# Optimization experiments

Hardware: AMD Instinct MI355X
Metric: run time of the kernel (lower is better)

## Reference

```python
import jax, jax.numpy as jnp
import numpy as np

HIDDEN = 4096
FFN = 11008
N_HEADS = 32
HEAD_DIM = HIDDEN // N_HEADS
BATCH = 1
SEQLEN = 1024
PAST = 1024
ROPE_BASE = 10000.0
EPS = 1e-6


def rms_norm(x, w, eps=EPS):
    var = jnp.mean(x * x, axis=-1, keepdims=True)
    return x * jax.lax.rsqrt(var + eps) * w


def rope(x):
    # x: (b, h, s, d); concatenated-halves variant: [e*cos - o*sin, e*sin + o*cos]
    s, d = x.shape[-2], x.shape[-1]
    pos = jnp.arange(s, dtype=x.dtype)[:, None]                      # (s, 1)
    freqs = ROPE_BASE ** (-jnp.arange(0, d, 2, dtype=x.dtype) / d)   # (d/2,)
    ang = pos * freqs                                                # (s, d/2)
    cos, sin = jnp.cos(ang), jnp.sin(ang)
    xe, xo = x[..., ::2], x[..., 1::2]
    return jnp.concatenate([xe * cos - xo * sin, xe * sin + xo * cos], axis=-1)


def setup_inputs() -> dict:
    key = jax.random.key(0)
    ks = jax.random.split(key, 9)
    sc = 0.02
    return {
        "x": jax.random.normal(ks[0], (BATCH, SEQLEN, HIDDEN), jnp.float32),
        "wq": jax.random.normal(ks[1], (HIDDEN, HIDDEN), jnp.float32) * sc,
        "wk": jax.random.normal(ks[2], (HIDDEN, HIDDEN), jnp.float32) * sc,
        "wv": jax.random.normal(ks[3], (HIDDEN, HIDDEN), jnp.float32) * sc,
        "wo": jax.random.normal(ks[4], (HIDDEN, HIDDEN), jnp.float32) * sc,
        "w1": jax.random.normal(ks[5], (FFN, HIDDEN), jnp.float32) * sc,
        "w2": jax.random.normal(ks[6], (HIDDEN, FFN), jnp.float32) * sc,
        "w3": jax.random.normal(ks[7], (FFN, HIDDEN), jnp.float32) * sc,
        "attn_norm_w": jnp.ones((HIDDEN,), jnp.float32),
        "ffn_norm_w": jnp.ones((HIDDEN,), jnp.float32),
        "past_k": jnp.zeros((BATCH, N_HEADS, PAST, HEAD_DIM), jnp.float32),
        "past_v": jnp.zeros((BATCH, N_HEADS, PAST, HEAD_DIM), jnp.float32),
    }


def reference(x, wq, wk, wv, wo, w1, w2, w3, attn_norm_w, ffn_norm_w, past_k, past_v):
    bsz, seqlen, _ = x.shape
    h = rms_norm(x, attn_norm_w)
    # projections: nn.Linear -> h @ W^T, reshape to (b, n_heads, s, d)
    def split_heads(y):
        return y.reshape(bsz, seqlen, N_HEADS, HEAD_DIM).transpose(0, 2, 1, 3)
    xq = split_heads(h @ wq.T)
    xk = split_heads(h @ wk.T)
    xv = split_heads(h @ wv.T)
    xq = rope(xq)
    xk = rope(xk)  # computed but unused downstream (faithful to source)
    # attention against the KV-cache buffers (zeros); no scaling, no mask
    scores_raw = jnp.einsum('bhsd,bhpd->bhsp', xq, past_k)
    scores = jax.nn.softmax(scores_raw, axis=-1)
    out = jnp.einsum('bhsp,bhpd->bhsd', scores, past_v)
    out = out.transpose(0, 2, 1, 3).reshape(bsz, seqlen, -1)
    xo = out @ wo.T
    # SwiGLU FFN (no residuals in source)
    hf = rms_norm(xo, ffn_norm_w)
    x1 = hf @ w1.T
    x3 = jax.nn.silu(hf @ w3.T)
    return (x1 * x3) @ w2.T
```

## Files before the change

kernel.cpp:

```cpp
#include <hip/hip_runtime.h>
#include <hip/hip_bf16.h>


typedef __attribute__((ext_vector_type(4))) float  floatx4;
typedef __attribute__((ext_vector_type(8))) __bf16 bf16x8;
typedef __attribute__((ext_vector_type(4))) __bf16 bf16x4;

#define HIDDEN 4096
#define FFN    11008
#define SEQLEN 1024
#define NHEADS 32
#define HDIM   128
#define PAST   1024

__global__ __launch_bounds__(256) void rmsnorm_bf16(
    const float* __restrict__ x, const float* __restrict__ w,
    __bf16* __restrict__ out)
{
    const int row = blockIdx.x;
    const float* xr = x + (size_t)row * HIDDEN;
    float4 v[4];
    float ss = 0.f;
#pragma unroll
    for (int i = 0; i < 4; ++i) {
        v[i] = *(const float4*)(xr + threadIdx.x * 4 + i * 1024);
        ss += v[i].x * v[i].x + v[i].y * v[i].y + v[i].z * v[i].z + v[i].w * v[i].w;
    }
#pragma unroll
    for (int off = 32; off > 0; off >>= 1) ss += __shfl_down(ss, off);
    __shared__ float red[4];
    if ((threadIdx.x & 63) == 0) red[threadIdx.x >> 6] = ss;
    __syncthreads();
    float total = red[0] + red[1] + red[2] + red[3];
    float scale = rsqrtf(total * (1.f / HIDDEN) + 1e-6f);
#pragma unroll
    for (int i = 0; i < 4; ++i) {
        int idx = threadIdx.x * 4 + i * 1024;
        float4 wv = *(const float4*)(w + idx);
        bf16x4 o;
        o[0] = (__bf16)(v[i].x * scale * wv.x);
        o[1] = (__bf16)(v[i].y * scale * wv.y);
        o[2] = (__bf16)(v[i].z * scale * wv.z);
        o[3] = (__bf16)(v[i].w * scale * wv.w);
        *(bf16x4*)(out + (size_t)row * HIDDEN + idx) = o;
    }
}

__global__ __launch_bounds__(256) void gemm_bt(
    const __bf16* __restrict__ A, const float* __restrict__ W,
    float* __restrict__ C, int M, int N, int K)
{
    __shared__ __bf16 As[128][40];
    __shared__ __bf16 Bs[128][40];

    const int tid  = threadIdx.x;
    const int bn   = blockIdx.x;
    const int bm   = blockIdx.y;
    const int wave = tid >> 6;
    const int lane = tid & 63;
    const int wr   = wave >> 1;
    const int wc   = wave & 1;
    const int lrow = lane & 15;
    const int quad = lane >> 4;

    floatx4 acc[4][4] = {};

    for (int k0 = 0; k0 < K; k0 += 32) {
#pragma unroll
        for (int i = 0; i < 2; ++i) {
            int id = tid + i * 256;
            int r = id >> 2, cc = id & 3;
            bf16x8 av = *(const bf16x8*)(A + (size_t)(bm * 128 + r) * K + k0 + cc * 8);
            *(bf16x8*)(&As[r][cc * 8]) = av;
        }
#pragma unroll
        for (int i = 0; i < 4; ++i) {
            int id = tid + i * 256;
            int r = id >> 3, cc = id & 7;
            float4 wv = *(const float4*)(W + (size_t)(bn * 128 + r) * K + k0 + cc * 4);
            bf16x4 bv;
            bv[0] = (__bf16)wv.x; bv[1] = (__bf16)wv.y;
            bv[2] = (__bf16)wv.z; bv[3] = (__bf16)wv.w;
            *(bf16x4*)(&Bs[r][cc * 4]) = bv;
        }
        __syncthreads();

        bf16x8 af[4], bfr[4];
#pragma unroll
        for (int i = 0; i < 4; ++i)
            af[i] = *(const bf16x8*)(&As[wr * 64 + i * 16 + lrow][quad * 8]);
#pragma unroll
        for (int j = 0; j < 4; ++j)
            bfr[j] = *(const bf16x8*)(&Bs[wc * 64 + j * 16 + lrow][quad * 8]);
#pragma unroll
        for (int i = 0; i < 4; ++i)
#pragma unroll
            for (int j = 0; j < 4; ++j)
                acc[i][j] = __builtin_amdgcn_mfma_f32_16x16x32_bf16(af[i], bfr[j], acc[i][j], 0, 0, 0);
        __syncthreads();
    }

#pragma unroll
    for (int i = 0; i < 4; ++i) {
        int mrow = bm * 128 + wr * 64 + i * 16 + quad * 4;
#pragma unroll
        for (int j = 0; j < 4; ++j) {
            int ncol = bn * 128 + wc * 64 + j * 16 + lrow;
            float* cp = C + (size_t)mrow * N + ncol;
#pragma unroll
            for (int r = 0; r < 4; ++r)
                cp[(size_t)r * N] = acc[i][j][r];
        }
    }
}

__global__ __launch_bounds__(256) void rope_cast(
    const float* __restrict__ xq, __bf16* __restrict__ outq)
{
    const int s = blockIdx.x;
    const float* row = xq + (size_t)s * HIDDEN;
    __bf16* orow = outq + (size_t)s * HIDDEN;
    for (int idx = threadIdx.x; idx < HIDDEN; idx += 256) {
        int d = idx & 127;
        int j = d & 63;
        int base = idx - d;
        float xe = row[base + 2 * j];
        float xo = row[base + 2 * j + 1];
        float freq = __powf(10000.f, -(float)(2 * j) * (1.f / 128.f));
        float sn, cs;
        __sincosf((float)s * freq, &sn, &cs);
        float v = (d < 64) ? (xe * cs - xo * sn) : (xe * sn + xo * cs);
        orow[idx] = (__bf16)v;
    }
}

__global__ __launch_bounds__(256) void attn_flash(
    const __bf16* __restrict__ q, const float* __restrict__ pk,
    const float* __restrict__ pv, __bf16* __restrict__ out)
{
    const int qt = blockIdx.x;
    const int h  = blockIdx.y;
    const int s0 = qt * 64;
    const int tid  = threadIdx.x;
    const int wave = tid >> 6;
    const int lane = tid & 63;
    const int l15  = lane & 15;
    const int quad = lane >> 4;

    __shared__ __bf16 Ks[64 * 136];
    __shared__ __bf16 Vt[128 * 72];
    __shared__ __bf16 Ps[64 * 72];

    bf16x8 qf[4];
    {
        const __bf16* qrow = q + (size_t)(s0 + wave * 16 + l15) * HIDDEN + h * HDIM;
#pragma unroll
        for (int ks = 0; ks < 4; ++ks)
            qf[ks] = *(const bf16x8*)(qrow + ks * 32 + quad * 8);
    }

    floatx4 Oa[8] = {};
    float m_r[4], l_r[4];
#pragma unroll
    for (int r = 0; r < 4; ++r) { m_r[r] = -1e30f; l_r[r] = 0.f; }

    for (int p0 = 0; p0 < PAST; p0 += 64) {
        const float* kbase = pk + ((size_t)h * PAST + p0) * HDIM;
        const float* vbase = pv + ((size_t)h * PAST + p0) * HDIM;
#pragma unroll
        for (int i = 0; i < 8; ++i) {
            int f = i * 256 + tid;
            int p = f >> 5, dq = (f & 31) * 4;
            float4 k4 = *(const float4*)(kbase + p * HDIM + dq);
            bf16x4 kb;
            kb[0] = (__bf16)k4.x; kb[1] = (__bf16)k4.y;
            kb[2] = (__bf16)k4.z; kb[3] = (__bf16)k4.w;
            *(bf16x4*)(&Ks[p * 136 + dq]) = kb;
            float4 v4 = *(const float4*)(vbase + p * HDIM + dq);
            Vt[(dq + 0) * 72 + p] = (__bf16)v4.x;
            Vt[(dq + 1) * 72 + p] = (__bf16)v4.y;
            Vt[(dq + 2) * 72 + p] = (__bf16)v4.z;
            Vt[(dq + 3) * 72 + p] = (__bf16)v4.w;
        }
        __syncthreads();

        floatx4 Sa[4] = {};
#pragma unroll
        for (int nb = 0; nb < 4; ++nb)
#pragma unroll
            for (int ks = 0; ks < 4; ++ks) {
                bf16x8 kf = *(const bf16x8*)(&Ks[(nb * 16 + l15) * 136 + ks * 32 + quad * 8]);
                Sa[nb] = __builtin_amdgcn_mfma_f32_16x16x32_bf16(qf[ks], kf, Sa[nb], 0, 0, 0);
            }

        float mnew[4];
#pragma unroll
        for (int r = 0; r < 4; ++r) {
            float t = fmaxf(fmaxf(Sa[0][r], Sa[1][r]), fmaxf(Sa[2][r], Sa[3][r]));
#pragma unroll
            for (int off = 1; off < 16; off <<= 1) t = fmaxf(t, __shfl_xor(t, off));
            mnew[r] = fmaxf(m_r[r], t);
        }
#pragma unroll
        for (int r = 0; r < 4; ++r) {
            float alpha = __expf(m_r[r] - mnew[r]);
            m_r[r] = mnew[r];
            float s = 0.f;
#pragma unroll
            for (int nb = 0; nb < 4; ++nb) {
                float e = __expf(Sa[nb][r] - mnew[r]);
                Sa[nb][r] = e;
                s += e;
            }
#pragma unroll
            for (int off = 1; off < 16; off <<= 1) s += __shfl_xor(s, off);
            l_r[r] = l_r[r] * alpha + s;
#pragma unroll
            for (int nb = 0; nb < 8; ++nb) Oa[nb][r] *= alpha;
        }

#pragma unroll
        for (int nb = 0; nb < 4; ++nb)
#pragma unroll
            for (int r = 0; r < 4; ++r)
                Ps[(wave * 16 + quad * 4 + r) * 72 + nb * 16 + l15] = (__bf16)Sa[nb][r];

#pragma unroll
        for (int ks2 = 0; ks2 < 2; ++ks2) {
            bf16x8 pf = *(const bf16x8*)(&Ps[(wave * 16 + l15) * 72 + ks2 * 32 + quad * 8]);
#pragma unroll
            for (int nb = 0; nb < 8; ++nb) {
                bf16x8 vf = *(const bf16x8*)(&Vt[(nb * 16 + l15) * 72 + ks2 * 32 + quad * 8]);
                Oa[nb] = __builtin_amdgcn_mfma_f32_16x16x32_bf16(pf, vf, Oa[nb], 0, 0, 0);
            }
        }
        __syncthreads();
    }

    float inv[4];
#pragma unroll
    for (int r = 0; r < 4; ++r) inv[r] = 1.f / l_r[r];
#pragma unroll
    for (int nb = 0; nb < 8; ++nb)
#pragma unroll
        for (int r = 0; r < 4; ++r)
            out[(size_t)(s0 + wave * 16 + quad * 4 + r) * HIDDEN + h * HDIM + nb * 16 + l15] =
                (__bf16)(Oa[nb][r] * inv[r]);
}

__global__ __launch_bounds__(256) void silu_mul_bf16(
    const float* __restrict__ x1, const float* __restrict__ x3,
    __bf16* __restrict__ out)
{
    int i = (blockIdx.x * 256 + threadIdx.x) * 4;
    float4 a = *(const float4*)(x1 + i);
    float4 b = *(const float4*)(x3 + i);
    bf16x4 o;
    o[0] = (__bf16)(a.x * (b.x / (1.f + __expf(-b.x))));
    o[1] = (__bf16)(a.y * (b.y / (1.f + __expf(-b.y))));
    o[2] = (__bf16)(a.z * (b.z / (1.f + __expf(-b.z))));
    o[3] = (__bf16)(a.w * (b.w / (1.f + __expf(-b.w))));
    *(bf16x4*)(out + i) = o;
}

extern "C" void kernel_launch(void* const* d_in, const int* in_sizes, int n_in,
                              void* d_out, int out_size, void* d_ws, size_t ws_size,
                              hipStream_t stream)
{
    const float* x   = (const float*)d_in[0];
    const float* wq  = (const float*)d_in[1];
    const float* wo  = (const float*)d_in[4];
    const float* w1  = (const float*)d_in[5];
    const float* w2  = (const float*)d_in[6];
    const float* w3  = (const float*)d_in[7];
    const float* anw = (const float*)d_in[8];
    const float* fnw = (const float*)d_in[9];
    const float* pk  = (const float*)d_in[10];
    const float* pv  = (const float*)d_in[11];
    float* out = (float*)d_out;

    char* ws = (char*)d_ws;
    constexpr size_t MB = 1ull << 20;
    __bf16* h_bf  = (__bf16*)(ws);
    float*  xq    = (float*)(ws + 8 * MB);
    __bf16* xq_bf = (__bf16*)(ws + 24 * MB);
    __bf16* ao_bf = (__bf16*)(ws + 32 * MB);
    float*  xo    = (float*)(ws + 40 * MB);
    __bf16* hf_bf = (__bf16*)(ws + 56 * MB);
    float*  x1    = (float*)(ws + 64 * MB);
    float*  x3    = (float*)(ws + 108 * MB);
    __bf16* g_bf  = (__bf16*)(ws + 152 * MB);

    rmsnorm_bf16<<<SEQLEN, 256, 0, stream>>>(x, anw, h_bf);
    gemm_bt<<<dim3(HIDDEN / 128, SEQLEN / 128), 256, 0, stream>>>(h_bf, wq, xq, SEQLEN, HIDDEN, HIDDEN);
    rope_cast<<<SEQLEN, 256, 0, stream>>>(xq, xq_bf);
    attn_flash<<<dim3(SEQLEN / 64, NHEADS), 256, 0, stream>>>(xq_bf, pk, pv, ao_bf);
    gemm_bt<<<dim3(HIDDEN / 128, SEQLEN / 128), 256, 0, stream>>>(ao_bf, wo, xo, SEQLEN, HIDDEN, HIDDEN);
    rmsnorm_bf16<<<SEQLEN, 256, 0, stream>>>(xo, fnw, hf_bf);
    gemm_bt<<<dim3(FFN / 128, SEQLEN / 128), 256, 0, stream>>>(hf_bf, w1, x1, SEQLEN, FFN, HIDDEN);
    gemm_bt<<<dim3(FFN / 128, SEQLEN / 128), 256, 0, stream>>>(hf_bf, w3, x3, SEQLEN, FFN, HIDDEN);
    silu_mul_bf16<<<(SEQLEN * FFN) / 1024, 256, 0, stream>>>(x1, x3, g_bf);
    gemm_bt<<<dim3(HIDDEN / 128, SEQLEN / 128), 256, 0, stream>>>(g_bf, w2, out, SEQLEN, HIDDEN, FFN);
}
```

Baseline: 1.682 ms.

## Double-buffer GEMM with direct-to-LDS loads, split-K, XCD remap, and RoPE table

Replaces the GEMM kernel with a K=64, double-buffered version. The A tile streams straight into LDS through global_load_lds with an XOR swizzle, while the next W tile is prefetched into registers during the MFMA work. Workgroups are remapped across XCDs. The 4096-wide GEMMs use a two-way split-K, and new combine kernels sum the partials (fused with RoPE for Q). RoPE sin/cos is precomputed into a table. The split-K path adds extra fp32 partial writes and reads in exchange for more parallelism and better latency hiding.

```diff
diff --git a/kernel.cpp b/kernel.cpp
--- a/kernel.cpp
+++ b/kernel.cpp
@@ -12,6 +12,12 @@
 #define NHEADS 32
 #define HDIM   128
 #define PAST   1024
+
+__device__ __forceinline__ void gload_lds16(const void* g, void* l) {
+    __builtin_amdgcn_global_load_lds(
+        (const __attribute__((address_space(1))) void*)g,
+        (__attribute__((address_space(3))) void*)l, 16, 0, 0);
+}
 
 __global__ __launch_bounds__(256) void rmsnorm_bf16(
     const float* __restrict__ x, const float* __restrict__ w,
@@ -46,92 +52,171 @@
     }
 }
 
-__global__ __launch_bounds__(256) void gemm_bt(
+template<int SPLIT>
+__global__ __launch_bounds__(256, 2) void gemm2(
     const __bf16* __restrict__ A, const float* __restrict__ W,
     float* __restrict__ C, int M, int N, int K)
 {
-    __shared__ __bf16 As[128][40];
-    __shared__ __bf16 Bs[128][40];
+    __shared__ __bf16 Asb[2][128 * 64];
+    __shared__ __bf16 Bsb[2][128 * 72];
 
     const int tid  = threadIdx.x;
-    const int bn   = blockIdx.x;
-    const int bm   = blockIdx.y;
     const int wave = tid >> 6;
     const int lane = tid & 63;
+    const int l15  = lane & 15;
+    const int quad = lane >> 4;
     const int wr   = wave >> 1;
     const int wc   = wave & 1;
-    const int lrow = lane & 15;
-    const int quad = lane >> 4;
+
+    const int nwg = gridDim.x;
+    int flat = blockIdx.x;
+    int q = nwg >> 3, r = nwg & 7;
+    int xcd = flat & 7, ii = flat >> 3;
+    int nf = (xcd < r) ? (xcd * (q + 1) + ii) : (r * (q + 1) + (xcd - r) * q + ii);
+    const int gm = M >> 7;
+    const int bn = nf / gm, bm = nf - bn * gm;
+
+    const int Kper  = K / SPLIT;
+    const int kbase = blockIdx.y * Kper;
+    const int nt    = Kper >> 6;
+
+    const int arow = (lane >> 3);
+    const int akb  = ((lane & 7) * 16) ^ ((lane >> 3) << 4);
+    const __bf16* Abase = A + (size_t)(bm * 128) * K + kbase + (akb >> 1);
+
+    const int wrow = tid >> 1, wh = tid & 1;
+    const float* Wbase = W + (size_t)(bn * 128 + wrow) * K + kbase + wh * 32;
 
     floatx4 acc[4][4] = {};
-
-    for (int k0 = 0; k0 < K; k0 += 32) {
-#pragma unroll
-        for (int i = 0; i < 2; ++i) {
-            int id = tid + i * 256;
-            int r = id >> 2, cc = id & 3;
-            bf16x8 av = *(const bf16x8*)(A + (size_t)(bm * 128 + r) * K + k0 + cc * 8);
-            *(bf16x8*)(&As[r][cc * 8]) = av;
-        }
+    float4 wreg[8];
+
+    {
+#pragma unroll
+        for (int j = 0; j < 8; ++j)
+            wreg[j] = *(const float4*)(Wbase + j * 4);
 #pragma unroll
         for (int i = 0; i < 4; ++i) {
-            int id = tid + i * 256;
-            int r = id >> 3, cc = id & 7;
-            float4 wv = *(const float4*)(W + (size_t)(bn * 128 + r) * K + k0 + cc * 4);
-            bf16x4 bv;
-            bv[0] = (__bf16)wv.x; bv[1] = (__bf16)wv.y;
-            bv[2] = (__bf16)wv.z; bv[3] = (__bf16)wv.w;
-            *(bf16x4*)(&Bs[r][cc * 4]) = bv;
+            int c = wave * 4 + i;
+            gload_lds16(Abase + (size_t)(c * 8 + arow) * K, &Asb[0][c * 512]);
+        }
+#pragma unroll
+        for (int j = 0; j < 4; ++j) {
+            bf16x8 b;
+            b[0] = (__bf16)wreg[2*j].x;   b[1] = (__bf16)wreg[2*j].y;
+            b[2] = (__bf16)wreg[2*j].z;   b[3] = (__bf16)wreg[2*j].w;
+            b[4] = (__bf16)wreg[2*j+1].x; b[5] = (__bf16)wreg[2*j+1].y;
+            b[6] = (__bf16)wreg[2*j+1].z; b[7] = (__bf16)wreg[2*j+1].w;
+            *(bf16x8*)(&Bsb[0][wrow * 72 + wh * 32 + j * 8]) = b;
         }
         __syncthreads();
-
-        bf16x8 af[4], bfr[4];
-#pragma unroll
-        for (int i = 0; i < 4; ++i)
-            af[i] = *(const bf16x8*)(&As[wr * 64 + i * 16 + lrow][quad * 8]);
-#pragma unroll
-        for (int j = 0; j < 4; ++j)
-            bfr[j] = *(const bf16x8*)(&Bs[wc * 64 + j * 16 + lrow][quad * 8]);
-#pragma unroll
-        for (int i = 0; i < 4; ++i)
-#pragma unroll
-            for (int j = 0; j < 4; ++j)
-                acc[i][j] = __builtin_amdgcn_mfma_f32_16x16x32_bf16(af[i], bfr[j], acc[i][j], 0, 0, 0);
-        __syncthreads();
-    }
-
+    }
+
+    for (int t = 0; t < nt; ++t) {
+        const int cur = t & 1, nxt = cur ^ 1;
+        const bool more = (t + 1 < nt);
+
+        if (more) {
+            const float* wb = Wbase + (t + 1) * 64;
+#pragma unroll
+            for (int j = 0; j < 8; ++j)
+                wreg[j] = *(const float4*)(wb + j * 4);
+            const __bf16* ab = Abase + (t + 1) * 64;
+#pragma unroll
+            for (int i = 0; i < 4; ++i) {
+                int c = wave * 4 + i;
+                gload_lds16(ab + (size_t)(c * 8 + arow) * K, &Asb[nxt][c * 512]);
+            }
+        }
+
+#pragma unroll
+        for (int kk = 0; kk < 2; ++kk) {
+            bf16x8 af[4], bfr[4];
+#pragma unroll
+            for (int i = 0; i < 4; ++i) {
+                int R  = wr * 64 + i * 16 + l15;
+                int kb = (kk * 64 + quad * 16) ^ ((l15 & 7) << 4);
+                af[i] = *(const bf16x8*)((const char*)&Asb[cur][R * 64] + kb);
+            }
+#pragma unroll
+            for (int j = 0; j < 4; ++j) {
+                int R2 = wc * 64 + j * 16 + l15;
+                bfr[j] = *(const bf16x8*)(&Bsb[cur][R2 * 72 + kk * 32 + quad * 8]);
+            }
+#pragma unroll
+            for (int i = 0; i < 4; ++i)
+#pragma unroll
+                for (int j = 0; j < 4; ++j)
+                    acc[i][j] = __builtin_amdgcn_mfma_f32_16x16x32_bf16(af[i], bfr[j], acc[i][j], 0, 0, 0);
+        }
+
+        if (more) {
+#pragma unroll
+            for (int j = 0; j < 4; ++j) {
+                bf16x8 b;
+                b[0] = (__bf16)wreg[2*j].x;   b[1] = (__bf16)wreg[2*j].y;
+                b[2] = (__bf16)wreg[2*j].z;   b[3] = (__bf16)wreg[2*j].w;
+                b[4] = (__bf16)wreg[2*j+1].x; b[5] = (__bf16)wreg[2*j+1].y;
+                b[6] = (__bf16)wreg[2*j+1].z; b[7] = (__bf16)wreg[2*j+1].w;
+                *(bf16x8*)(&Bsb[nxt][wrow * 72 + wh * 32 + j * 8]) = b;
+            }
+            __syncthreads();
+        }
+    }
+
+    float* Co = (SPLIT > 1) ? (C + (size_t)blockIdx.y * M * N) : C;
 #pragma unroll
     for (int i = 0; i < 4; ++i) {
         int mrow = bm * 128 + wr * 64 + i * 16 + quad * 4;
 #pragma unroll
         for (int j = 0; j < 4; ++j) {
-            int ncol = bn * 128 + wc * 64 + j * 16 + lrow;
-            float* cp = C + (size_t)mrow * N + ncol;
-#pragma unroll
-            for (int r = 0; r < 4; ++r)
-                cp[(size_t)r * N] = acc[i][j][r];
-        }
-    }
-}
-
-__global__ __launch_bounds__(256) void rope_cast(
-    const float* __restrict__ xq, __bf16* __restrict__ outq)
+            int ncol = bn * 128 + wc * 64 + j * 16 + l15;
+            float* cp = Co + (size_t)mrow * N + ncol;
+#pragma unroll
+            for (int rr = 0; rr < 4; ++rr)
+                cp[(size_t)rr * N] = acc[i][j][rr];
+        }
+    }
+}
+
+__global__ __launch_bounds__(256) void rope_table(float* __restrict__ tab)
+{
+    int idx = blockIdx.x * 256 + threadIdx.x;
+    int s = idx >> 6, j = idx & 63;
+    float freq = __powf(10000.f, -(float)(2 * j) * (1.f / 128.f));
+    float sn, cs;
+    __sincosf((float)s * freq, &sn, &cs);
+    tab[2 * idx]     = cs;
+    tab[2 * idx + 1] = sn;
+}
+
+__global__ __launch_bounds__(256) void combine_rope(
+    const float* __restrict__ p, const float* __restrict__ tab,
+    __bf16* __restrict__ out)
 {
     const int s = blockIdx.x;
-    const float* row = xq + (size_t)s * HIDDEN;
-    __bf16* orow = outq + (size_t)s * HIDDEN;
-    for (int idx = threadIdx.x; idx < HIDDEN; idx += 256) {
-        int d = idx & 127;
-        int j = d & 63;
-        int base = idx - d;
-        float xe = row[base + 2 * j];
-        float xo = row[base + 2 * j + 1];
-        float freq = __powf(10000.f, -(float)(2 * j) * (1.f / 128.f));
-        float sn, cs;
-        __sincosf((float)s * freq, &sn, &cs);
-        float v = (d < 64) ? (xe * cs - xo * sn) : (xe * sn + xo * cs);
-        orow[idx] = (__bf16)v;
-    }
+    const float* r0 = p + (size_t)s * HIDDEN;
+    const float* r1 = r0 + (size_t)SEQLEN * HIDDEN;
+    __bf16* orow = out + (size_t)s * HIDDEN;
+    for (int pi = threadIdx.x; pi < 2048; pi += 256) {
+        int h = pi >> 6, j = pi & 63;
+        int base = h * 128;
+        float2 e0 = *(const float2*)(r0 + base + 2 * j);
+        float2 e1 = *(const float2*)(r1 + base + 2 * j);
+        float xe = e0.x + e1.x, xo = e0.y + e1.y;
+        float2 cs = *(const float2*)(tab + (size_t)s * 128 + 2 * j);
+        orow[base + j]      = (__bf16)(xe * cs.x - xo * cs.y);
+        orow[base + 64 + j] = (__bf16)(xe * cs.y + xo * cs.x);
+    }
+}
+
+__global__ __launch_bounds__(256) void combine_add(
+    const float* __restrict__ p, float* __restrict__ out, int n)
+{
+    int i = (blockIdx.x * 256 + threadIdx.x) * 4;
+    float4 a = *(const float4*)(p + i);
+    float4 b = *(const float4*)(p + n + i);
+    float4 o; o.x = a.x + b.x; o.y = a.y + b.y; o.z = a.z + b.z; o.w = a.w + b.w;
+    *(float4*)(out + i) = o;
 }
 
 __global__ __launch_bounds__(256) void attn_flash(
@@ -280,25 +365,37 @@
     float* out = (float*)d_out;
 
     char* ws = (char*)d_ws;
-    constexpr size_t MB = 1ull << 20;
-    __bf16* h_bf  = (__bf16*)(ws);
-    float*  xq    = (float*)(ws + 8 * MB);
-    __bf16* xq_bf = (__bf16*)(ws + 24 * MB);
-    __bf16* ao_bf = (__bf16*)(ws + 32 * MB);
-    float*  xo    = (float*)(ws + 40 * MB);
-    __bf16* hf_bf = (__bf16*)(ws + 56 * MB);
-    float*  x1    = (float*)(ws + 64 * MB);
-    float*  x3    = (float*)(ws + 108 * MB);
-    __bf16* g_bf  = (__bf16*)(ws + 152 * MB);
-
+    constexpr size_t MB  = 1ull << 20;
+    constexpr size_t HMB = 512ull << 10;
+    float*  tab   = (float*)(ws);
+    __bf16* h_bf  = (__bf16*)(ws + HMB);
+    float*  qp    = (float*)(ws + HMB + 8  * MB);
+    __bf16* xq_bf = (__bf16*)(ws + HMB);
+    __bf16* ao_bf = (__bf16*)(ws + HMB + 8  * MB);
+    float*  op    = (float*)(ws + HMB + 16 * MB);
+    float*  xo    = (float*)(ws + HMB);
+    __bf16* hf_bf = (__bf16*)(ws + HMB + 48 * MB);
+    float*  x1    = (float*)(ws + HMB);
+    float*  x3    = (float*)(ws + HMB + 56 * MB);
+    __bf16* g_bf  = (__bf16*)(ws + HMB + 102 * MB);
+    float*  w2p   = (float*)(ws + HMB);
+
+    rope_table<<<256, 256, 0, stream>>>(tab);
     rmsnorm_bf16<<<SEQLEN, 256, 0, stream>>>(x, anw, h_bf);
-    gemm_bt<<<dim3(HIDDEN / 128, SEQLEN / 128), 256, 0, stream>>>(h_bf, wq, xq, SEQLEN, HIDDEN, HIDDEN);
-    rope_cast<<<SEQLEN, 256, 0, stream>>>(xq, xq_bf);
+    gemm2<2><<<dim3((HIDDEN / 128) * (SEQLEN / 128), 2), 256, 0, stream>>>(
+        h_bf, wq, qp, SEQLEN, HIDDEN, HIDDEN);
+    combine_rope<<<SEQLEN, 256, 0, stream>>>(qp, tab, xq_bf);
     attn_flash<<<dim3(SEQLEN / 64, NHEADS), 256, 0, stream>>>(xq_bf, pk, pv, ao_bf);
-    gemm_bt<<<dim3(HIDDEN / 128, SEQLEN / 128), 256, 0, stream>>>(ao_bf, wo, xo, SEQLEN, HIDDEN, HIDDEN);
+    gemm2<2><<<dim3((HIDDEN / 128) * (SEQLEN / 128), 2), 256, 0, stream>>>(
+        ao_bf, wo, op, SEQLEN, HIDDEN, HIDDEN);
+    combine_add<<<(SEQLEN * HIDDEN) / 1024, 256, 0, stream>>>(op, xo, SEQLEN * HIDDEN);
     rmsnorm_bf16<<<SEQLEN, 256, 0, stream>>>(xo, fnw, hf_bf);
-    gemm_bt<<<dim3(FFN / 128, SEQLEN / 128), 256, 0, stream>>>(hf_bf, w1, x1, SEQLEN, FFN, HIDDEN);
-    gemm_bt<<<dim3(FFN / 128, SEQLEN / 128), 256, 0, stream>>>(hf_bf, w3, x3, SEQLEN, FFN, HIDDEN);
+    gemm2<1><<<dim3((FFN / 128) * (SEQLEN / 128), 1), 256, 0, stream>>>(
+        hf_bf, w1, x1, SEQLEN, FFN, HIDDEN);
+    gemm2<1><<<dim3((FFN / 128) * (SEQLEN / 128), 1), 256, 0, stream>>>(
+        hf_bf, w3, x3, SEQLEN, FFN, HIDDEN);
     silu_mul_bf16<<<(SEQLEN * FFN) / 1024, 256, 0, stream>>>(x1, x3, g_bf);
-    gemm_bt<<<dim3(HIDDEN / 128, SEQLEN / 128), 256, 0, stream>>>(g_bf, w2, out, SEQLEN, HIDDEN, FFN);
-}
+    gemm2<2><<<dim3((HIDDEN / 128) * (SEQLEN / 128), 2), 256, 0, stream>>>(
+        g_bf, w2, w2p, SEQLEN, HIDDEN, FFN);
+    combine_add<<<(SEQLEN * HIDDEN) / 1024, 256, 0, stream>>>(w2p, out, SEQLEN * HIDDEN);
+}
```

New measurement: 1.619 ms. 1.04x faster.
